# Kernel optimization log

Hardware: AMD Instinct MI355X
Metric: run time of the kernel (lower is better)

Reference implementation:

```python
import jax, jax.numpy as jnp
import numpy as np

B, IN_F, K_INT, OUT_F = 256, 512, 75, 64
INIT = 0.05


def setup_inputs() -> dict:
    key = jax.random.key(0)
    k_x, k_t = jax.random.split(key)
    x = jax.random.normal(k_x, (B, IN_F), dtype=jnp.float32)
    T = jax.random.normal(k_t, (IN_F, K_INT, OUT_F), dtype=jnp.float32) * INIT
    return {"x": x, "T": T}


def reference(x, T):
    # M: [B, K, O] = x @ T flattened over (K, O)
    Bn = x.shape[0]
    M = (x @ T.reshape(T.shape[0], -1)).reshape(Bn, T.shape[1], T.shape[2])
    # pairwise L1 distance over K: [B, B, O]
    # (original materializes [B, B, K, O] broadcasted diff; same math)
    M_diff = M[None, :, :, :] - M[:, None, :, :]
    distance = jnp.abs(M_diff).sum(axis=2)           # [B, B, O]
    exp_distance = jnp.exp(-distance)                # [B, B, O]
    minibatch_features = exp_distance.sum(axis=1) - 1.0  # [B, O]; -1 removes self-distance
    return minibatch_features
```

## Files before the change

kernel.cpp:

```cpp
#include <hip/hip_runtime.h>


typedef __attribute__((ext_vector_type(8))) short bf16x8;
typedef __attribute__((ext_vector_type(4))) float f32x4;
typedef unsigned short u16;
typedef unsigned int u32;

__device__ inline u16 f2bf(float f) {
  u32 u = __float_as_uint(f);
  return (u16)((u + 0x7FFFu + ((u >> 16) & 1u)) >> 16);
}
__device__ inline float bflo(u32 u) { return __uint_as_float(u << 16); }
__device__ inline float bfhi(u32 u) { return __uint_as_float(u & 0xFFFF0000u); }

__global__ __launch_bounds__(256) void cvt_all(const float* __restrict__ x,
                                               const float* __restrict__ T,
                                               u16* __restrict__ xb,
                                               u16* __restrict__ Tb) {
  const int bid = blockIdx.x;
  const int tid = threadIdx.x;

  if (bid >= 600) {
    const int i = (bid - 600) * 256 + tid;
    const float4* x4 = reinterpret_cast<const float4*>(x);
    const float4 v0 = x4[i * 2], v1 = x4[i * 2 + 1];
    uint4 o;
    o.x = (u32)f2bf(v0.x) | ((u32)f2bf(v0.y) << 16);
    o.y = (u32)f2bf(v0.z) | ((u32)f2bf(v0.w) << 16);
    o.z = (u32)f2bf(v1.x) | ((u32)f2bf(v1.y) << 16);
    o.w = (u32)f2bf(v1.z) | ((u32)f2bf(v1.w) << 16);
    *reinterpret_cast<uint4*>(xb + i * 8) = o;
    return;
  }

  const int f0 = (bid & 7) << 6;
  const int k = bid >> 3;
  __shared__ float tile[64][65];

  const float4* T4 = reinterpret_cast<const float4*>(T);
  const int r = tid >> 2;
  const int c = tid & 3;
#pragma unroll
  for (int h = 0; h < 4; ++h) {
    const int q = c + (h << 2);
    const float4 v = T4[(f0 + r) * 1200 + k * 16 + q];
    tile[r][(q << 2) + 0] = v.x;
    tile[r][(q << 2) + 1] = v.y;
    tile[r][(q << 2) + 2] = v.z;
    tile[r][(q << 2) + 3] = v.w;
  }
  __syncthreads();

  const int w = tid >> 2;
  u16 us[16];
#pragma unroll
  for (int j = 0; j < 16; ++j) us[j] = f2bf(tile[(c << 4) + j][w]);
  uint4 p0, p1;
  p0.x = (u32)us[0] | ((u32)us[1] << 16);
  p0.y = (u32)us[2] | ((u32)us[3] << 16);
  p0.z = (u32)us[4] | ((u32)us[5] << 16);
  p0.w = (u32)us[6] | ((u32)us[7] << 16);
  p1.x = (u32)us[8] | ((u32)us[9] << 16);
  p1.y = (u32)us[10] | ((u32)us[11] << 16);
  p1.z = (u32)us[12] | ((u32)us[13] << 16);
  p1.w = (u32)us[14] | ((u32)us[15] << 16);
  uint4* dst = reinterpret_cast<uint4*>(Tb + ((k << 6) + w) * 512 + f0 + (c << 4));
  dst[0] = p0;
  dst[1] = p1;
}

__global__ __launch_bounds__(256) void md_gemm_mfma(const u16* __restrict__ Tb,
                                                    const u16* __restrict__ xb,
                                                    float* __restrict__ Mt2) {
  const int tid = threadIdx.x;
  const int l = tid & 63, w = tid >> 6;
  const int n0 = (blockIdx.x << 6) + ((w >> 1) << 5);
  const int b0 = (blockIdx.y << 6) + ((w & 1) << 5);
  const int z = blockIdx.z;
  const int lr = l & 15;
  const int ko = (l >> 4) << 3;

  const u16* pa0 = Tb + (n0 + lr) * 512 + z * 256 + ko;
  const u16* pa1 = pa0 + 16 * 512;
  const u16* pb0 = xb + (b0 + lr) * 512 + z * 256 + ko;
  const u16* pb1 = pb0 + 16 * 512;

  f32x4 d00 = {0.f, 0.f, 0.f, 0.f}, d01 = d00, d10 = d00, d11 = d00;

#pragma unroll 4
  for (int kk = 0; kk < 8; ++kk) {
    const int off = kk << 5;
    const bf16x8 a0 = *reinterpret_cast<const bf16x8*>(pa0 + off);
    const bf16x8 a1 = *reinterpret_cast<const bf16x8*>(pa1 + off);
    const bf16x8 f0 = *reinterpret_cast<const bf16x8*>(pb0 + off);
    const bf16x8 f1 = *reinterpret_cast<const bf16x8*>(pb1 + off);
    d00 = __builtin_amdgcn_mfma_f32_16x16x32_bf16(a0, f0, d00, 0, 0, 0);
    d01 = __builtin_amdgcn_mfma_f32_16x16x32_bf16(a0, f1, d01, 0, 0, 0);
    d10 = __builtin_amdgcn_mfma_f32_16x16x32_bf16(a1, f0, d10, 0, 0, 0);
    d11 = __builtin_amdgcn_mfma_f32_16x16x32_bf16(a1, f1, d11, 0, 0, 0);
  }

  float* Mt = Mt2 + z * 1228800;
#pragma unroll
  for (int r = 0; r < 4; ++r) {
    const int row = ((l >> 4) << 2) + r;
    {
      const int n = n0 + row;
      float* base = Mt + (n & 63) * 19200 + (n >> 6) * 256;
      base[b0 + lr] = d00[r];
      base[b0 + 16 + lr] = d01[r];
    }
    {
      const int n = n0 + 16 + row;
      float* base = Mt + (n & 63) * 19200 + (n >> 6) * 256;
      base[b0 + lr] = d10[r];
      base[b0 + 16 + lr] = d11[r];
    }
  }
}

__global__ __launch_bounds__(512) void md_pair4(const float* __restrict__ Mt2,
                                                float* __restrict__ out) {
  const int bid = blockIdx.x;
  const int o = bid & 63;
  const int it = bid >> 6;
  const int ibase = it << 5;
  const int tid = threadIdx.x;
  const int is = tid & 15;
  const int jg = tid >> 4;

  __shared__ alignas(16) u16 MjB[38 * 256];
  __shared__ alignas(16) float MiF[38 * 32];

  const float* M0 = Mt2 + o * 19200;
  const float* M1 = M0 + 1228800;

  float d[2][8];
#pragma unroll
  for (int a = 0; a < 2; ++a)
#pragma unroll
    for (int b = 0; b < 8; ++b) d[a][b] = 0.0f;

  for (int h = 0; h < 2; ++h) {
    const int kbase = h * 38;
    __syncthreads();
    for (int idx = tid; idx < 38 * 64; idx += 512) {
      const int kk = idx >> 6, q = idx & 63;
      const int gk = kbase + kk;
      uint2 p;
      if (gk < 75) {
        const int goff = gk * 256 + (q << 2);
        const float4 v0 = *reinterpret_cast<const float4*>(M0 + goff);
        const float4 v1 = *reinterpret_cast<const float4*>(M1 + goff);
        p.x = (u32)f2bf(v0.x + v1.x) | ((u32)f2bf(v0.y + v1.y) << 16);
        p.y = (u32)f2bf(v0.z + v1.z) | ((u32)f2bf(v0.w + v1.w) << 16);
      } else {
        p = make_uint2(0u, 0u);
      }
      *reinterpret_cast<uint2*>(MjB + kk * 256 + (q << 2)) = p;
    }
    for (int idx = tid; idx < 38 * 32; idx += 512) {
      const int kk = idx >> 5, ii = idx & 31;
      const int gk = kbase + kk;
      const int goff = gk * 256 + ibase + ii;
      MiF[kk * 32 + ii] = (gk < 75) ? (M0[goff] + M1[goff]) : 0.0f;
    }
    __syncthreads();

#pragma unroll 19
    for (int kk = 0; kk < 38; ++kk) {
      const float2 vi = *reinterpret_cast<const float2*>(MiF + kk * 32 + (is << 1));
      const uint4 ju = *reinterpret_cast<const uint4*>(MjB + kk * 256 + (jg << 3));
      const float ja[8] = {bflo(ju.x), bfhi(ju.x), bflo(ju.y), bfhi(ju.y),
                           bflo(ju.z), bfhi(ju.z), bflo(ju.w), bfhi(ju.w)};
#pragma unroll
      for (int b = 0; b < 8; ++b) {
        d[0][b] += __builtin_fabsf(ja[b] - vi.x);
        d[1][b] += __builtin_fabsf(ja[b] - vi.y);
      }
    }
  }

  float s[2];
#pragma unroll
  for (int a = 0; a < 2; ++a) {
    const int ia = ibase + (is << 1) + a;
    float t = 0.0f;
#pragma unroll
    for (int b = 0; b < 8; ++b) {
      const int j = (jg << 3) + b;
      const float e = __expf(-d[a][b]);
      t += (j == ia) ? 0.0f : e;
    }
    s[a] = t;
  }

  __syncthreads();
  float* red = reinterpret_cast<float*>(MjB);
  red[((is << 1) + 0) * 33 + jg] = s[0];
  red[((is << 1) + 1) * 33 + jg] = s[1];
  __syncthreads();
  if (tid < 32) {
    float t = 0.0f;
#pragma unroll
    for (int g = 0; g < 32; ++g) t += red[tid * 33 + g];
    out[(ibase + tid) * 64 + o] = t;
  }
}

extern "C" void kernel_launch(void* const* d_in, const int* in_sizes, int n_in,
                              void* d_out, int out_size, void* d_ws, size_t ws_size,
                              hipStream_t stream) {
  const float* x = (const float*)d_in[0];
  const float* T = (const float*)d_in[1];
  float* out = (float*)d_out;

  char* ws = (char*)d_ws;
  float* Mt2 = (float*)ws;
  u16* Tb = (u16*)(ws + 9830400);
  u16* xb = (u16*)(ws + 14745600);

  cvt_all<<<664, 256, 0, stream>>>(x, T, xb, Tb);
  md_gemm_mfma<<<dim3(75, 4, 2), 256, 0, stream>>>(Tb, xb, Mt2);
  md_pair4<<<512, 512, 0, stream>>>(Mt2, out);
}
```

Measured before the change: 54.22 us.

## Fuse bf16 conversion into GEMM loads and drop the separate convert kernel

Removes the cvt_all pre-pass, which transposed T and converted x and T to bf16 through workspace. The GEMM now reads fp32 x and T directly and converts in registers by truncating to bf16. This saves a kernel launch and a full write-and-reread of the converted operands. In exchange, the T loads become strided scalar loads (stride 4800 floats along the reduction dim), though consecutive lanes still read adjacent addresses. Truncation replaces round-to-nearest, which slightly changes numerics.

```diff
diff --git a/kernel.cpp b/kernel.cpp
--- a/kernel.cpp
+++ b/kernel.cpp
@@ -10,90 +10,48 @@
   u32 u = __float_as_uint(f);
   return (u16)((u + 0x7FFFu + ((u >> 16) & 1u)) >> 16);
 }
+__device__ inline short bftrunc(float f) {
+  return (short)(__float_as_uint(f) >> 16);
+}
 __device__ inline float bflo(u32 u) { return __uint_as_float(u << 16); }
 __device__ inline float bfhi(u32 u) { return __uint_as_float(u & 0xFFFF0000u); }
 
-__global__ __launch_bounds__(256) void cvt_all(const float* __restrict__ x,
-                                               const float* __restrict__ T,
-                                               u16* __restrict__ xb,
-                                               u16* __restrict__ Tb) {
-  const int bid = blockIdx.x;
-  const int tid = threadIdx.x;
-
-  if (bid >= 600) {
-    const int i = (bid - 600) * 256 + tid;
-    const float4* x4 = reinterpret_cast<const float4*>(x);
-    const float4 v0 = x4[i * 2], v1 = x4[i * 2 + 1];
-    uint4 o;
-    o.x = (u32)f2bf(v0.x) | ((u32)f2bf(v0.y) << 16);
-    o.y = (u32)f2bf(v0.z) | ((u32)f2bf(v0.w) << 16);
-    o.z = (u32)f2bf(v1.x) | ((u32)f2bf(v1.y) << 16);
-    o.w = (u32)f2bf(v1.z) | ((u32)f2bf(v1.w) << 16);
-    *reinterpret_cast<uint4*>(xb + i * 8) = o;
-    return;
-  }
-
-  const int f0 = (bid & 7) << 6;
-  const int k = bid >> 3;
-  __shared__ float tile[64][65];
-
-  const float4* T4 = reinterpret_cast<const float4*>(T);
-  const int r = tid >> 2;
-  const int c = tid & 3;
-#pragma unroll
-  for (int h = 0; h < 4; ++h) {
-    const int q = c + (h << 2);
-    const float4 v = T4[(f0 + r) * 1200 + k * 16 + q];
-    tile[r][(q << 2) + 0] = v.x;
-    tile[r][(q << 2) + 1] = v.y;
-    tile[r][(q << 2) + 2] = v.z;
-    tile[r][(q << 2) + 3] = v.w;
-  }
-  __syncthreads();
-
-  const int w = tid >> 2;
-  u16 us[16];
-#pragma unroll
-  for (int j = 0; j < 16; ++j) us[j] = f2bf(tile[(c << 4) + j][w]);
-  uint4 p0, p1;
-  p0.x = (u32)us[0] | ((u32)us[1] << 16);
-  p0.y = (u32)us[2] | ((u32)us[3] << 16);
-  p0.z = (u32)us[4] | ((u32)us[5] << 16);
-  p0.w = (u32)us[6] | ((u32)us[7] << 16);
-  p1.x = (u32)us[8] | ((u32)us[9] << 16);
-  p1.y = (u32)us[10] | ((u32)us[11] << 16);
-  p1.z = (u32)us[12] | ((u32)us[13] << 16);
-  p1.w = (u32)us[14] | ((u32)us[15] << 16);
-  uint4* dst = reinterpret_cast<uint4*>(Tb + ((k << 6) + w) * 512 + f0 + (c << 4));
-  dst[0] = p0;
-  dst[1] = p1;
-}
-
-__global__ __launch_bounds__(256) void md_gemm_mfma(const u16* __restrict__ Tb,
-                                                    const u16* __restrict__ xb,
-                                                    float* __restrict__ Mt2) {
+__global__ __launch_bounds__(256) void md_gemm_direct(const float* __restrict__ x,
+                                                      const float* __restrict__ T,
+                                                      float* __restrict__ Mt2) {
   const int tid = threadIdx.x;
   const int l = tid & 63, w = tid >> 6;
-  const int n0 = (blockIdx.x << 6) + ((w >> 1) << 5);
+  const int bx = blockIdx.x;
   const int b0 = (blockIdx.y << 6) + ((w & 1) << 5);
   const int z = blockIdx.z;
   const int lr = l & 15;
   const int ko = (l >> 4) << 3;
+  const int oh = (w >> 1) << 5;
 
-  const u16* pa0 = Tb + (n0 + lr) * 512 + z * 256 + ko;
-  const u16* pa1 = pa0 + 16 * 512;
-  const u16* pb0 = xb + (b0 + lr) * 512 + z * 256 + ko;
-  const u16* pb1 = pb0 + 16 * 512;
+  const float* At = T + (z * 256 + ko) * 4800 + bx * 64 + oh + lr;
+  const float* Bx0 = x + (b0 + lr) * 512 + z * 256 + ko;
+  const float* Bx1 = Bx0 + 16 * 512;
 
   f32x4 d00 = {0.f, 0.f, 0.f, 0.f}, d01 = d00, d10 = d00, d11 = d00;
 
-#pragma unroll 4
+#pragma unroll 2
   for (int kk = 0; kk < 8; ++kk) {
-    const int off = kk << 5;
-    const bf16x8 a0 = *reinterpret_cast<const bf16x8*>(pa0 + off);
-    const bf16x8 a1 = *reinterpret_cast<const bf16x8*>(pa1 + off);
-    const bf16x8 f0 = *reinterpret_cast<const bf16x8*>(pb0 + off);
-    const bf16x8 f1 = *reinterpret_cast<const bf16x8*>(pb1 + off);
+    bf16x8 a0, a1, f0, f1;
+    const float* Ak = At + (kk << 5) * 4800;
+#pragma unroll
+    for (int e = 0; e < 8; ++e) {
+      a0[e] = bftrunc(Ak[e * 4800]);
+      a1[e] = bftrunc(Ak[e * 4800 + 16]);
+    }
+    const float4 b00 = *reinterpret_cast<const float4*>(Bx0 + (kk << 5));
+    const float4 b01 = *reinterpret_cast<const float4*>(Bx0 + (kk << 5) + 4);
+    const float4 b10 = *reinterpret_cast<const float4*>(Bx1 + (kk << 5));
+    const float4 b11 = *reinterpret_cast<const float4*>(Bx1 + (kk << 5) + 4);
+    f0[0] = bftrunc(b00.x); f0[1] = bftrunc(b00.y); f0[2] = bftrunc(b00.z); f0[3] = bftrunc(b00.w);
+    f0[4] = bftrunc(b01.x); f0[5] = bftrunc(b01.y); f0[6] = bftrunc(b01.z); f0[7] = bftrunc(b01.w);
+    f1[0] = bftrunc(b10.x); f1[1] = bftrunc(b10.y); f1[2] = bftrunc(b10.z); f1[3] = bftrunc(b10.w);
+    f1[4] = bftrunc(b11.x); f1[5] = bftrunc(b11.y); f1[6] = bftrunc(b11.z); f1[7] = bftrunc(b11.w);
+
     d00 = __builtin_amdgcn_mfma_f32_16x16x32_bf16(a0, f0, d00, 0, 0, 0);
     d01 = __builtin_amdgcn_mfma_f32_16x16x32_bf16(a0, f1, d01, 0, 0, 0);
     d10 = __builtin_amdgcn_mfma_f32_16x16x32_bf16(a1, f0, d10, 0, 0, 0);
@@ -101,6 +59,7 @@
   }
 
   float* Mt = Mt2 + z * 1228800;
+  const int n0 = (bx << 6) + oh;
 #pragma unroll
   for (int r = 0; r < 4; ++r) {
     const int row = ((l >> 4) << 2) + r;
@@ -215,12 +174,8 @@
   const float* T = (const float*)d_in[1];
   float* out = (float*)d_out;
 
-  char* ws = (char*)d_ws;
-  float* Mt2 = (float*)ws;
-  u16* Tb = (u16*)(ws + 9830400);
-  u16* xb = (u16*)(ws + 14745600);
+  float* Mt2 = (float*)d_ws;
 
-  cvt_all<<<664, 256, 0, stream>>>(x, T, xb, Tb);
-  md_gemm_mfma<<<dim3(75, 4, 2), 256, 0, stream>>>(Tb, xb, Mt2);
+  md_gemm_direct<<<dim3(75, 4, 2), 256, 0, stream>>>(x, T, Mt2);
   md_pair4<<<512, 512, 0, stream>>>(Mt2, out);
 }
```

New measurement: 50.35 us. 1.08x faster.
